# Performance work log

Measured on AMD Instinct MI355X. Metric: run time of the kernel, lower is better.

The kernel has to match this reference:

```python
import math
import jax, jax.numpy as jnp
import numpy as np

B, Q, HID = 4, 4, 4096
NH, NKV, HD = 32, 8, 128
GROUPS = NH // NKV
CACHE_LEN = 4096
CACHE_MAX = CACHE_LEN + 512  # prefill_len + max_len(512)
ROPE_THETA = 500000.0
SCALE = 1.0 / math.sqrt(128.0)  # hardcoded softmax_scale in module


def rotate_half(x):
    x1, x2 = jnp.split(x, 2, axis=-1)
    return jnp.concatenate([-x2, x1], axis=-1)


def setup_inputs() -> dict:
    key = jax.random.key(0)
    ks = jax.random.split(key, 8)
    std = 0.02
    # RoPE angles for positions [CACHE_LEN, CACHE_LEN+Q)
    pos = (CACHE_LEN + jnp.arange(Q)).astype(jnp.float32)
    inv_freq = 1.0 / (ROPE_THETA ** (jnp.arange(0, HD, 2, dtype=jnp.float32) / HD))
    freqs = pos[:, None] * inv_freq[None, :]            # [Q, HD/2]
    emb = jnp.concatenate([freqs, freqs], axis=-1)      # [Q, HD]
    cos = jnp.broadcast_to(jnp.cos(emb)[None], (B, Q, HD)).astype(jnp.float32)
    sin = jnp.broadcast_to(jnp.sin(emb)[None], (B, Q, HD)).astype(jnp.float32)
    return {
        "hidden_states": jax.random.normal(ks[0], (B, Q, HID), jnp.float32),
        "cos": cos,
        "sin": sin,
        "K_Cache": jax.random.normal(ks[1], (B, NKV, CACHE_MAX, HD), jnp.float32) * 0.5,
        "V_Cache": jax.random.normal(ks[2], (B, NKV, CACHE_MAX, HD), jnp.float32) * 0.5,
        "Wq": jax.random.normal(ks[3], (NH * HD, HID), jnp.float32) * std,
        "Wk": jax.random.normal(ks[4], (NKV * HD, HID), jnp.float32) * std,
        "Wv": jax.random.normal(ks[5], (NKV * HD, HID), jnp.float32) * std,
        "Wo": jax.random.normal(ks[6], (HID, NH * HD), jnp.float32) * std,
        "cache_lens": int(CACHE_LEN),
    }


def reference(hidden_states, cos, sin, K_Cache, V_Cache, Wq, Wk, Wv, Wo, cache_lens):
    b, q, _ = hidden_states.shape
    # projections (torch Linear: x @ W.T), reshape to [b, h, q, d]
    qs = jnp.einsum('bsh,oh->bso', hidden_states, Wq).reshape(b, q, NH, HD).transpose(0, 2, 1, 3)
    ks = jnp.einsum('bsh,oh->bso', hidden_states, Wk).reshape(b, q, NKV, HD).transpose(0, 2, 1, 3)
    vs = jnp.einsum('bsh,oh->bso', hidden_states, Wv).reshape(b, q, NKV, HD).transpose(0, 2, 1, 3)
    # RoPE, unsqueeze_dim=1 (head axis)
    c, s = cos[:, None, :, :], sin[:, None, :, :]
    qs = qs * c + rotate_half(qs) * s
    ks = ks * c + rotate_half(ks) * s
    # scatter new K/V into the cache at offset cache_lens
    K_Cache = K_Cache.at[:, :, cache_lens:cache_lens + q, :].set(ks)
    V_Cache = V_Cache.at[:, :, cache_lens:cache_lens + q, :].set(vs)
    # K_total/V_total = cache prefix ++ fresh keys/values; GQA repeat
    K_total = jnp.repeat(jnp.concatenate([K_Cache[:, :, :cache_lens, :], ks], axis=2), GROUPS, axis=1)
    V_total = jnp.repeat(jnp.concatenate([V_Cache[:, :, :cache_lens, :], vs], axis=2), GROUPS, axis=1)
    scores = jnp.einsum('bhqd,bhkd->bhqk', qs, K_total) * SCALE
    # causal mask over the appended q tokens, cache prefix fully visible
    tri = jnp.triu(jnp.ones((q, q), bool), 1)
    mask = jnp.concatenate([jnp.zeros((q, cache_lens), bool), tri], axis=1)
    scores = jnp.where(mask[None, None], -jnp.inf, scores)
    attn = jax.nn.softmax(scores.astype(jnp.float32), axis=-1).astype(V_total.dtype)
    out = jnp.einsum('bhqk,bhkd->bhqd', attn, V_total)
    out = out.transpose(0, 2, 1, 3).reshape(b, q, NH * HD)
    return jnp.einsum('bsh,oh->bso', out, Wo)
```

## Files before the change

### kernel.cpp

```cpp
#include <hip/hip_runtime.h>
#include <math.h>

#define HIDK 4096
#define NHQ 32
#define HD 128
#define CMAX 4608
#define CLEN 4096
#define NCH 32
#define SCALE 0.08838834764831845f

__device__ __forceinline__ float4 ld4(const float* p) { return *reinterpret_cast<const float4*>(p); }
__device__ __forceinline__ float dot4(float4 a, float4 b) { return a.x*b.x + a.y*b.y + a.z*b.z + a.w*b.w; }
__device__ __forceinline__ int swz(int row, int colf) { return row * 128 + (colf ^ ((row & 31) << 2)); }

__global__ __launch_bounds__(256) void gemm3_kernel(
    const float* __restrict__ X,
    const float* __restrict__ W1, const float* __restrict__ W2, const float* __restrict__ W3,
    int n1, int n2,
    float* __restrict__ o1, int os1,
    float* __restrict__ o2, int os2,
    float* __restrict__ o3, int os3)
{
  __shared__ float Xs[2][16][256];

  const int tid = threadIdx.x, lane = tid & 63, w = tid >> 6;
  const int o = blockIdx.x * 8 + w * 2;

  const float* Wb; float* ob; int os;
  if (o < n1)           { Wb = W1 + (size_t)o * HIDK;            ob = o1 + o;            os = os1; }
  else if (o < n1 + n2) { const int f = o - n1;      Wb = W2 + (size_t)f * HIDK; ob = o2 + f; os = os2; }
  else                  { const int f = o - n1 - n2; Wb = W3 + (size_t)f * HIDK; ob = o3 + f; os = os3; }

  const int xr = tid >> 6;
  const int sr = tid >> 4;
  (void)xr; (void)sr;

  const int strow = tid >> 6;
  const int stcol = (tid & 63) * 4;

  float acc0[16], acc1[16];
  #pragma unroll
  for (int b = 0; b < 16; ++b) { acc0[b] = 0.f; acc1[b] = 0.f; }

  #pragma unroll
  for (int j = 0; j < 4; ++j)
    *(float4*)&Xs[0][strow + j * 4][stcol] = ld4(X + (size_t)(strow + j * 4) * HIDK + stcol);

  int cur = 0;
  #pragma unroll 2
  for (int kt = 0; kt < 16; ++kt) {
    const float4 w0 = ld4(Wb + (size_t)kt * 256 + lane * 4);
    const float4 w1 = ld4(Wb + HIDK + (size_t)kt * 256 + lane * 4);
    float4 g[4];
    if (kt < 15) {
      #pragma unroll
      for (int j = 0; j < 4; ++j)
        g[j] = ld4(X + (size_t)(strow + j * 4) * HIDK + (kt + 1) * 256 + stcol);
    }
    __syncthreads();
    #pragma unroll
    for (int b = 0; b < 16; ++b) {
      const float4 x4 = *(const float4*)&Xs[cur][b][lane * 4];
      acc0[b] += dot4(x4, w0);
      acc1[b] += dot4(x4, w1);
    }
    if (kt < 15) {
      #pragma unroll
      for (int j = 0; j < 4; ++j)
        *(float4*)&Xs[cur ^ 1][strow + j * 4][stcol] = g[j];
    }
    cur ^= 1;
  }

  #pragma unroll
  for (int m = 1; m < 64; m <<= 1)
    #pragma unroll
    for (int b = 0; b < 16; ++b) {
      acc0[b] += __shfl_xor(acc0[b], m, 64);
      acc1[b] += __shfl_xor(acc1[b], m, 64);
    }
  if (lane == 0) {
    #pragma unroll
    for (int b = 0; b < 16; ++b) {
      ob[(size_t)b * os]     = acc0[b];
      ob[(size_t)b * os + 1] = acc1[b];
    }
  }
}

__global__ __launch_bounds__(256) void attn2_kernel(
    const float* __restrict__ qraw, const float* __restrict__ Kc, const float* __restrict__ Vc,
    const float* __restrict__ cosp, const float* __restrict__ sinp,
    float* __restrict__ partO, float* __restrict__ partM, float* __restrict__ partL)
{
  __shared__ float qsh[16][128];
  __shared__ float KV[64 * 128];
  __shared__ float P[128][20];

  const int tid = threadIdx.x, lane = tid & 63, w = tid >> 6;
  const int chunk = blockIdx.x & 31, bkv = blockIdx.x >> 5;
  const int b = bkv >> 3, kv = bkv & 7;
  const int p0 = chunk * 128;

  const float* Kbase = Kc + ((size_t)(b * 8 + kv) * CMAX + p0) * HD;
  const float* Vbase = Vc + ((size_t)(b * 8 + kv) * CMAX + p0) * HD;
  const int c0 = (tid & 31) * 4, r0 = tid >> 5;

  #pragma unroll
  for (int j = 0; j < 8; ++j) {
    const int e = tid + j * 256;
    const int r = e >> 7, d = e & 127;
    const int s = r & 3, hl = r >> 2;
    const float* qp = qraw + (size_t)(b * 4 + s) * HIDK + (kv * 4 + hl) * HD;
    const float c  = cosp[(b * 4 + s) * HD + d];
    const float sn = sinp[(b * 4 + s) * HD + d];
    const float sgn = (d < 64) ? -1.f : 1.f;
    qsh[r][d] = (qp[d] * c + sgn * qp[d ^ 64] * sn) * SCALE;
  }
  #pragma unroll
  for (int j = 0; j < 8; ++j) {
    const int r = r0 + j * 8;
    *(float4*)&KV[swz(r, c0)] = ld4(Kbase + (size_t)r * HD + c0);
  }
  __syncthreads();

  const int pos16 = lane & 15, quart = lane >> 4;
  const int prow = w * 16 + pos16;

  #pragma unroll
  for (int t = 0; t < 2; ++t) {
    float sc[16];
    #pragma unroll
    for (int r = 0; r < 16; ++r) sc[r] = 0.f;
    #pragma unroll
    for (int d4 = 0; d4 < 8; ++d4) {
      const int kcol = quart * 32 + d4 * 4;
      const float4 k4 = *(const float4*)&KV[swz(prow, kcol)];
      #pragma unroll
      for (int r = 0; r < 16; ++r)
        sc[r] += dot4(k4, *(const float4*)&qsh[r][kcol]);
    }
    #pragma unroll
    for (int r = 0; r < 16; ++r) {
      sc[r] += __shfl_xor(sc[r], 16, 64);
      sc[r] += __shfl_xor(sc[r], 32, 64);
    }
    if (lane < 16) {
      #pragma unroll
      for (int r = 0; r < 16; ++r) P[t * 64 + prow][r] = sc[r];
    }
    __syncthreads();
    if (t == 0) {
      #pragma unroll
      for (int j = 0; j < 8; ++j) {
        const int r = r0 + j * 8;
        *(float4*)&KV[swz(r, c0)] = ld4(Kbase + (size_t)(64 + r) * HD + c0);
      }
      __syncthreads();
    }
  }

  float4 g[8];
  #pragma unroll
  for (int j = 0; j < 8; ++j)
    g[j] = ld4(Vbase + (size_t)(r0 + j * 8) * HD + c0);

  #pragma unroll
  for (int rr = 0; rr < 4; ++rr) {
    const int r = w * 4 + rr;
    float v0 = P[lane][r], v1 = P[lane + 64][r];
    float mx = fmaxf(v0, v1);
    #pragma unroll
    for (int m = 1; m < 64; m <<= 1) mx = fmaxf(mx, __shfl_xor(mx, m, 64));
    v0 = __expf(v0 - mx);
    v1 = __expf(v1 - mx);
    P[lane][r] = v0;
    P[lane + 64][r] = v1;
    float l = v0 + v1;
    #pragma unroll
    for (int m = 1; m < 64; m <<= 1) l += __shfl_xor(l, m, 64);
    if (lane == 0) {
      const int row = (b * NHQ + kv * 4 + (r >> 2)) * 4 + (r & 3);
      partM[row * NCH + chunk] = mx;
      partL[row * NCH + chunk] = l;
    }
  }
  #pragma unroll
  for (int j = 0; j < 8; ++j)
    *(float4*)&KV[swz(r0 + j * 8, c0)] = g[j];
  __syncthreads();

  const int ph = lane >> 5, vc0 = (lane & 31) * 4;
  float4 o[4];
  #pragma unroll
  for (int rr = 0; rr < 4; ++rr) o[rr] = make_float4(0.f, 0.f, 0.f, 0.f);

  #pragma unroll
  for (int t = 0; t < 2; ++t) {
    #pragma unroll 4
    for (int i = 0; i < 32; ++i) {
      const int pr = 2 * i + ph;
      const float4 v4 = *(const float4*)&KV[swz(pr, vc0)];
      const float4 p4 = *(const float4*)&P[t * 64 + pr][w * 4];
      o[0].x += p4.x * v4.x; o[0].y += p4.x * v4.y; o[0].z += p4.x * v4.z; o[0].w += p4.x * v4.w;
      o[1].x += p4.y * v4.x; o[1].y += p4.y * v4.y; o[1].z += p4.y * v4.z; o[1].w += p4.y * v4.w;
      o[2].x += p4.z * v4.x; o[2].y += p4.z * v4.y; o[2].z += p4.z * v4.z; o[2].w += p4.z * v4.w;
      o[3].x += p4.w * v4.x; o[3].y += p4.w * v4.y; o[3].z += p4.w * v4.z; o[3].w += p4.w * v4.w;
    }
    if (t == 0) {
      __syncthreads();
      #pragma unroll
      for (int j = 0; j < 8; ++j) {
        const int r = r0 + j * 8;
        *(float4*)&KV[swz(r, c0)] = ld4(Vbase + (size_t)(64 + r) * HD + c0);
      }
      __syncthreads();
    }
  }

  #pragma unroll
  for (int rr = 0; rr < 4; ++rr) {
    o[rr].x += __shfl_xor(o[rr].x, 32, 64);
    o[rr].y += __shfl_xor(o[rr].y, 32, 64);
    o[rr].z += __shfl_xor(o[rr].z, 32, 64);
    o[rr].w += __shfl_xor(o[rr].w, 32, 64);
  }
  if (lane < 32) {
    #pragma unroll
    for (int rr = 0; rr < 4; ++rr) {
      const int r = w * 4 + rr;
      const int row = (b * NHQ + kv * 4 + (r >> 2)) * 4 + (r & 3);
      *(float4*)&partO[((size_t)row * NCH + chunk) * HD + lane * 4] = o[rr];
    }
  }
}

__global__ __launch_bounds__(64) void combine_kernel(
    const float* __restrict__ qraw, const float* __restrict__ kraw, const float* __restrict__ vraw,
    const float* __restrict__ cosp, const float* __restrict__ sinp,
    const float* __restrict__ partO, const float* __restrict__ partM, const float* __restrict__ partL,
    float* __restrict__ attn)
{
  const int bid = blockIdx.x;
  const int s = bid & 3;
  const int h = (bid >> 2) & 31;
  const int b = bid >> 7;
  const int kv = h >> 2;
  const int lane = threadIdx.x;
  const int d0 = lane * 2;

  float M = -INFINITY;
  #pragma unroll 4
  for (int c = 0; c < NCH; ++c) M = fmaxf(M, partM[bid * NCH + c]);

  float qr0, qr1;
  {
    const float* qp = qraw + (size_t)(b * 4 + s) * HIDK + h * HD;
    const float c0 = cosp[(b * 4 + s) * HD + d0],     sn0 = sinp[(b * 4 + s) * HD + d0];
    const float c1 = cosp[(b * 4 + s) * HD + d0 + 1], sn1 = sinp[(b * 4 + s) * HD + d0 + 1];
    const float sg0 = (d0 < 64) ? -1.f : 1.f;
    const float sg1 = ((d0 + 1) < 64) ? -1.f : 1.f;
    qr0 = (qp[d0] * c0 + sg0 * qp[d0 ^ 64] * sn0) * SCALE;
    qr1 = (qp[d0 + 1] * c1 + sg1 * qp[(d0 + 1) ^ 64] * sn1) * SCALE;
  }

  float sj[4] = {0.f, 0.f, 0.f, 0.f};
  float Mp = M;
  #pragma unroll
  for (int j = 0; j < 4; ++j) {
    if (j <= s) {
      const float* kp = kraw + (size_t)(b * 4 + j) * 1024 + kv * HD;
      const float c0 = cosp[(b * 4 + j) * HD + d0],     sn0 = sinp[(b * 4 + j) * HD + d0];
      const float c1 = cosp[(b * 4 + j) * HD + d0 + 1], sn1 = sinp[(b * 4 + j) * HD + d0 + 1];
      const float sg0 = (d0 < 64) ? -1.f : 1.f;
      const float sg1 = ((d0 + 1) < 64) ? -1.f : 1.f;
      const float kr0 = kp[d0] * c0 + sg0 * kp[d0 ^ 64] * sn0;
      const float kr1 = kp[d0 + 1] * c1 + sg1 * kp[(d0 + 1) ^ 64] * sn1;
      float part = qr0 * kr0 + qr1 * kr1;
      #pragma unroll
      for (int m = 1; m < 64; m <<= 1) part += __shfl_xor(part, m, 64);
      sj[j] = part;
      Mp = fmaxf(Mp, part);
    }
  }

  float ltot = 0.f, O0 = 0.f, O1 = 0.f;
  #pragma unroll 4
  for (int c = 0; c < NCH; ++c) {
    const float a = __expf(partM[bid * NCH + c] - Mp);
    ltot += partL[bid * NCH + c] * a;
    const float2 v = *(const float2*)&partO[((size_t)bid * NCH + c) * HD + d0];
    O0 += a * v.x;
    O1 += a * v.y;
  }
  #pragma unroll
  for (int j = 0; j < 4; ++j) {
    if (j <= s) {
      const float e = __expf(sj[j] - Mp);
      ltot += e;
      const float* vp = vraw + (size_t)(b * 4 + j) * 1024 + kv * HD + d0;
      O0 += e * vp[0];
      O1 += e * vp[1];
    }
  }
  const float inv = 1.f / ltot;
  *(float2*)&attn[(size_t)(b * 4 + s) * HIDK + h * HD + d0] = make_float2(O0 * inv, O1 * inv);
}

extern "C" void kernel_launch(void* const* d_in, const int* in_sizes, int n_in,
                              void* d_out, int out_size, void* d_ws, size_t ws_size,
                              hipStream_t stream)
{
  const float* hid  = (const float*)d_in[0];
  const float* cosp = (const float*)d_in[1];
  const float* sinp = (const float*)d_in[2];
  const float* Kc   = (const float*)d_in[3];
  const float* Vc   = (const float*)d_in[4];
  const float* Wq   = (const float*)d_in[5];
  const float* Wk   = (const float*)d_in[6];
  const float* Wv   = (const float*)d_in[7];
  const float* Wo   = (const float*)d_in[8];
  float* out = (float*)d_out;

  float* ws    = (float*)d_ws;
  float* qraw  = ws;
  float* kraw  = ws + 65536;
  float* vraw  = ws + 81920;
  float* attn  = ws + 98304;
  float* partO = ws + 163840;
  float* partM = partO + (size_t)512 * NCH * 128;
  float* partL = partM + (size_t)512 * NCH;

  gemm3_kernel<<<768, 256, 0, stream>>>(hid, Wq, Wk, Wv, 4096, 1024,
                                        qraw, 4096, kraw, 1024, vraw, 1024);
  attn2_kernel<<<32 * NCH, 256, 0, stream>>>(qraw, Kc, Vc, cosp, sinp, partO, partM, partL);
  combine_kernel<<<512, 64, 0, stream>>>(qraw, kraw, vraw, cosp, sinp, partO, partM, partL, attn);
  gemm3_kernel<<<512, 256, 0, stream>>>(attn, Wo, Wo, Wo, 4096, 0,
                                        out, 4096, out, 4096, out, 4096);
}
```

Measured before the change: 136.3 us.

## Stream K/V directly from global in split-KV attention, prep rotated Q separately

Replaces the LDS-staged attention kernel with one where each wave reads K rows and V rows straight from global memory and keeps 16 query rows in registers. RoPE on Q moves into a separate prep kernel that writes a transposed, pre-scaled Q for broadcast reads, and the two waves merge their softmax partials in LDS. Partial outputs are stored in fp16 to halve partO traffic into the combine kernel. The costs are an extra launch, higher register pressure from 16 float4 accumulators, and reduced precision in the partial outputs.

```diff
diff --git a/kernel.cpp b/kernel.cpp
--- a/kernel.cpp
+++ b/kernel.cpp
@@ -1,4 +1,5 @@
 #include <hip/hip_runtime.h>
+#include <hip/hip_fp16.h>
 #include <math.h>
 
 #define HIDK 4096
@@ -11,7 +12,6 @@
 
 __device__ __forceinline__ float4 ld4(const float* p) { return *reinterpret_cast<const float4*>(p); }
 __device__ __forceinline__ float dot4(float4 a, float4 b) { return a.x*b.x + a.y*b.y + a.z*b.z + a.w*b.w; }
-__device__ __forceinline__ int swz(int row, int colf) { return row * 128 + (colf ^ ((row & 31) << 2)); }
 
 __global__ __launch_bounds__(256) void gemm3_kernel(
     const float* __restrict__ X,
@@ -31,10 +31,6 @@
   else if (o < n1 + n2) { const int f = o - n1;      Wb = W2 + (size_t)f * HIDK; ob = o2 + f; os = os2; }
   else                  { const int f = o - n1 - n2; Wb = W3 + (size_t)f * HIDK; ob = o3 + f; os = os3; }
 
-  const int xr = tid >> 6;
-  const int sr = tid >> 4;
-  (void)xr; (void)sr;
-
   const int strow = tid >> 6;
   const int stcol = (tid & 63) * 4;
 
@@ -88,157 +84,129 @@
   }
 }
 
-__global__ __launch_bounds__(256) void attn2_kernel(
-    const float* __restrict__ qraw, const float* __restrict__ Kc, const float* __restrict__ Vc,
-    const float* __restrict__ cosp, const float* __restrict__ sinp,
-    float* __restrict__ partO, float* __restrict__ partM, float* __restrict__ partL)
-{
-  __shared__ float qsh[16][128];
-  __shared__ float KV[64 * 128];
-  __shared__ float P[128][20];
+__global__ __launch_bounds__(256) void qt_prep_kernel(
+    const float* __restrict__ qraw, const float* __restrict__ cosp,
+    const float* __restrict__ sinp, float* __restrict__ qt)
+{
+  const int e = blockIdx.x * 256 + threadIdx.x;
+  const int r = e & 15;
+  const int d = (e >> 4) & 127;
+  const int bkv = e >> 11;
+  const int b = bkv >> 3, kv = bkv & 7;
+  const int s = r & 3, hl = r >> 2;
+  const float* qp = qraw + (size_t)(b * 4 + s) * HIDK + (kv * 4 + hl) * HD;
+  const float c  = cosp[(b * 4 + s) * HD + d];
+  const float sn = sinp[(b * 4 + s) * HD + d];
+  const float sgn = (d < 64) ? -1.f : 1.f;
+  qt[e] = (qp[d] * c + sgn * qp[d ^ 64] * sn) * SCALE;
+}
+
+__global__ __launch_bounds__(128) void attn3_kernel(
+    const float* __restrict__ qt, const float* __restrict__ Kc, const float* __restrict__ Vc,
+    __half* __restrict__ partOh, float* __restrict__ partM, float* __restrict__ partL)
+{
+  __shared__ float Plds[2][16][66];
+  __shared__ float Oex[16][132];
+  __shared__ float MLe[32];
 
   const int tid = threadIdx.x, lane = tid & 63, w = tid >> 6;
   const int chunk = blockIdx.x & 31, bkv = blockIdx.x >> 5;
   const int b = bkv >> 3, kv = bkv & 7;
-  const int p0 = chunk * 128;
-
-  const float* Kbase = Kc + ((size_t)(b * 8 + kv) * CMAX + p0) * HD;
-  const float* Vbase = Vc + ((size_t)(b * 8 + kv) * CMAX + p0) * HD;
-  const int c0 = (tid & 31) * 4, r0 = tid >> 5;
-
-  #pragma unroll
-  for (int j = 0; j < 8; ++j) {
-    const int e = tid + j * 256;
-    const int r = e >> 7, d = e & 127;
-    const int s = r & 3, hl = r >> 2;
-    const float* qp = qraw + (size_t)(b * 4 + s) * HIDK + (kv * 4 + hl) * HD;
-    const float c  = cosp[(b * 4 + s) * HD + d];
-    const float sn = sinp[(b * 4 + s) * HD + d];
-    const float sgn = (d < 64) ? -1.f : 1.f;
-    qsh[r][d] = (qp[d] * c + sgn * qp[d ^ 64] * sn) * SCALE;
-  }
-  #pragma unroll
-  for (int j = 0; j < 8; ++j) {
-    const int r = r0 + j * 8;
-    *(float4*)&KV[swz(r, c0)] = ld4(Kbase + (size_t)r * HD + c0);
+  const int p0 = chunk * 128 + w * 64;
+
+  const float* qtb = qt + (size_t)bkv * 2048;
+  const float* Kp  = Kc + ((size_t)bkv * CMAX + p0 + lane) * HD;
+
+  float sc[16];
+  #pragma unroll
+  for (int r = 0; r < 16; ++r) sc[r] = 0.f;
+  #pragma unroll 4
+  for (int d4 = 0; d4 < 32; ++d4) {
+    const float4 k4 = ld4(Kp + d4 * 4);
+    #pragma unroll
+    for (int r = 0; r < 16; ++r) sc[r] += k4.x * qtb[(d4 * 4 + 0) * 16 + r];
+    #pragma unroll
+    for (int r = 0; r < 16; ++r) sc[r] += k4.y * qtb[(d4 * 4 + 1) * 16 + r];
+    #pragma unroll
+    for (int r = 0; r < 16; ++r) sc[r] += k4.z * qtb[(d4 * 4 + 2) * 16 + r];
+    #pragma unroll
+    for (int r = 0; r < 16; ++r) sc[r] += k4.w * qtb[(d4 * 4 + 3) * 16 + r];
+  }
+
+  float m[16], l[16];
+  #pragma unroll
+  for (int r = 0; r < 16; ++r) {
+    float mx = sc[r];
+    #pragma unroll
+    for (int st = 1; st < 64; st <<= 1) mx = fmaxf(mx, __shfl_xor(mx, st, 64));
+    const float p = __expf(sc[r] - mx);
+    float ls = p;
+    #pragma unroll
+    for (int st = 1; st < 64; st <<= 1) ls += __shfl_xor(ls, st, 64);
+    m[r] = mx; l[r] = ls;
+    Plds[w][r][lane] = p;
+  }
+
+  const int dsub = lane & 31, par = lane >> 5;
+  const float* Vp = Vc + ((size_t)bkv * CMAX + p0 + par) * HD + dsub * 4;
+  float4 o[16];
+  #pragma unroll
+  for (int r = 0; r < 16; ++r) o[r] = make_float4(0.f, 0.f, 0.f, 0.f);
+  #pragma unroll 4
+  for (int i = 0; i < 32; ++i) {
+    const float4 v4 = ld4(Vp + (size_t)(2 * i) * HD);
+    #pragma unroll
+    for (int r = 0; r < 16; ++r) {
+      const float p = Plds[w][r][2 * i + par];
+      o[r].x += p * v4.x; o[r].y += p * v4.y; o[r].z += p * v4.z; o[r].w += p * v4.w;
+    }
+  }
+  #pragma unroll
+  for (int r = 0; r < 16; ++r) {
+    o[r].x += __shfl_xor(o[r].x, 32, 64);
+    o[r].y += __shfl_xor(o[r].y, 32, 64);
+    o[r].z += __shfl_xor(o[r].z, 32, 64);
+    o[r].w += __shfl_xor(o[r].w, 32, 64);
+  }
+
+  if (w == 1) {
+    if (lane < 32) {
+      #pragma unroll
+      for (int r = 0; r < 16; ++r) *(float4*)&Oex[r][dsub * 4] = o[r];
+    }
+    if (lane == 0) {
+      #pragma unroll
+      for (int r = 0; r < 16; ++r) { MLe[r] = m[r]; MLe[16 + r] = l[r]; }
+    }
   }
   __syncthreads();
-
-  const int pos16 = lane & 15, quart = lane >> 4;
-  const int prow = w * 16 + pos16;
-
-  #pragma unroll
-  for (int t = 0; t < 2; ++t) {
-    float sc[16];
-    #pragma unroll
-    for (int r = 0; r < 16; ++r) sc[r] = 0.f;
-    #pragma unroll
-    for (int d4 = 0; d4 < 8; ++d4) {
-      const int kcol = quart * 32 + d4 * 4;
-      const float4 k4 = *(const float4*)&KV[swz(prow, kcol)];
-      #pragma unroll
-      for (int r = 0; r < 16; ++r)
-        sc[r] += dot4(k4, *(const float4*)&qsh[r][kcol]);
-    }
+  if (w == 0 && lane < 32) {
     #pragma unroll
     for (int r = 0; r < 16; ++r) {
-      sc[r] += __shfl_xor(sc[r], 16, 64);
-      sc[r] += __shfl_xor(sc[r], 32, 64);
-    }
-    if (lane < 16) {
-      #pragma unroll
-      for (int r = 0; r < 16; ++r) P[t * 64 + prow][r] = sc[r];
-    }
-    __syncthreads();
-    if (t == 0) {
-      #pragma unroll
-      for (int j = 0; j < 8; ++j) {
-        const int r = r0 + j * 8;
-        *(float4*)&KV[swz(r, c0)] = ld4(Kbase + (size_t)(64 + r) * HD + c0);
+      const float m1 = MLe[r], l1 = MLe[16 + r];
+      const float M  = fmaxf(m[r], m1);
+      const float a0 = __expf(m[r] - M), a1 = __expf(m1 - M);
+      const float4 o1 = *(const float4*)&Oex[r][dsub * 4];
+      const float ox = a0 * o[r].x + a1 * o1.x;
+      const float oy = a0 * o[r].y + a1 * o1.y;
+      const float oz = a0 * o[r].z + a1 * o1.z;
+      const float ow = a0 * o[r].w + a1 * o1.w;
+      const int row = (b * NHQ + kv * 4 + (r >> 2)) * 4 + (r & 3);
+      const size_t idx = ((size_t)row * NCH + chunk) * HD + dsub * 4;
+      *(__half2*)&partOh[idx]     = __floats2half2_rn(ox, oy);
+      *(__half2*)&partOh[idx + 2] = __floats2half2_rn(oz, ow);
+      if (dsub == 0) {
+        partM[row * NCH + chunk] = M;
+        partL[row * NCH + chunk] = a0 * l[r] + a1 * l1;
       }
-      __syncthreads();
-    }
-  }
-
-  float4 g[8];
-  #pragma unroll
-  for (int j = 0; j < 8; ++j)
-    g[j] = ld4(Vbase + (size_t)(r0 + j * 8) * HD + c0);
-
-  #pragma unroll
-  for (int rr = 0; rr < 4; ++rr) {
-    const int r = w * 4 + rr;
-    float v0 = P[lane][r], v1 = P[lane + 64][r];
-    float mx = fmaxf(v0, v1);
-    #pragma unroll
-    for (int m = 1; m < 64; m <<= 1) mx = fmaxf(mx, __shfl_xor(mx, m, 64));
-    v0 = __expf(v0 - mx);
-    v1 = __expf(v1 - mx);
-    P[lane][r] = v0;
-    P[lane + 64][r] = v1;
-    float l = v0 + v1;
-    #pragma unroll
-    for (int m = 1; m < 64; m <<= 1) l += __shfl_xor(l, m, 64);
-    if (lane == 0) {
-      const int row = (b * NHQ + kv * 4 + (r >> 2)) * 4 + (r & 3);
-      partM[row * NCH + chunk] = mx;
-      partL[row * NCH + chunk] = l;
-    }
-  }
-  #pragma unroll
-  for (int j = 0; j < 8; ++j)
-    *(float4*)&KV[swz(r0 + j * 8, c0)] = g[j];
-  __syncthreads();
-
-  const int ph = lane >> 5, vc0 = (lane & 31) * 4;
-  float4 o[4];
-  #pragma unroll
-  for (int rr = 0; rr < 4; ++rr) o[rr] = make_float4(0.f, 0.f, 0.f, 0.f);
-
-  #pragma unroll
-  for (int t = 0; t < 2; ++t) {
-    #pragma unroll 4
-    for (int i = 0; i < 32; ++i) {
-      const int pr = 2 * i + ph;
-      const float4 v4 = *(const float4*)&KV[swz(pr, vc0)];
-      const float4 p4 = *(const float4*)&P[t * 64 + pr][w * 4];
-      o[0].x += p4.x * v4.x; o[0].y += p4.x * v4.y; o[0].z += p4.x * v4.z; o[0].w += p4.x * v4.w;
-      o[1].x += p4.y * v4.x; o[1].y += p4.y * v4.y; o[1].z += p4.y * v4.z; o[1].w += p4.y * v4.w;
-      o[2].x += p4.z * v4.x; o[2].y += p4.z * v4.y; o[2].z += p4.z * v4.z; o[2].w += p4.z * v4.w;
-      o[3].x += p4.w * v4.x; o[3].y += p4.w * v4.y; o[3].z += p4.w * v4.z; o[3].w += p4.w * v4.w;
-    }
-    if (t == 0) {
-      __syncthreads();
-      #pragma unroll
-      for (int j = 0; j < 8; ++j) {
-        const int r = r0 + j * 8;
-        *(float4*)&KV[swz(r, c0)] = ld4(Vbase + (size_t)(64 + r) * HD + c0);
-      }
-      __syncthreads();
-    }
-  }
-
-  #pragma unroll
-  for (int rr = 0; rr < 4; ++rr) {
-    o[rr].x += __shfl_xor(o[rr].x, 32, 64);
-    o[rr].y += __shfl_xor(o[rr].y, 32, 64);
-    o[rr].z += __shfl_xor(o[rr].z, 32, 64);
-    o[rr].w += __shfl_xor(o[rr].w, 32, 64);
-  }
-  if (lane < 32) {
-    #pragma unroll
-    for (int rr = 0; rr < 4; ++rr) {
-      const int r = w * 4 + rr;
-      const int row = (b * NHQ + kv * 4 + (r >> 2)) * 4 + (r & 3);
-      *(float4*)&partO[((size_t)row * NCH + chunk) * HD + lane * 4] = o[rr];
     }
   }
 }
 
 __global__ __launch_bounds__(64) void combine_kernel(
-    const float* __restrict__ qraw, const float* __restrict__ kraw, const float* __restrict__ vraw,
+    const float* __restrict__ qt, const float* __restrict__ kraw, const float* __restrict__ vraw,
     const float* __restrict__ cosp, const float* __restrict__ sinp,
-    const float* __restrict__ partO, const float* __restrict__ partM, const float* __restrict__ partL,
+    const __half* __restrict__ partOh, const float* __restrict__ partM, const float* __restrict__ partL,
     float* __restrict__ attn)
 {
   const int bid = blockIdx.x;
@@ -253,16 +221,9 @@
   #pragma unroll 4
   for (int c = 0; c < NCH; ++c) M = fmaxf(M, partM[bid * NCH + c]);
 
-  float qr0, qr1;
-  {
-    const float* qp = qraw + (size_t)(b * 4 + s) * HIDK + h * HD;
-    const float c0 = cosp[(b * 4 + s) * HD + d0],     sn0 = sinp[(b * 4 + s) * HD + d0];
-    const float c1 = cosp[(b * 4 + s) * HD + d0 + 1], sn1 = sinp[(b * 4 + s) * HD + d0 + 1];
-    const float sg0 = (d0 < 64) ? -1.f : 1.f;
-    const float sg1 = ((d0 + 1) < 64) ? -1.f : 1.f;
-    qr0 = (qp[d0] * c0 + sg0 * qp[d0 ^ 64] * sn0) * SCALE;
-    qr1 = (qp[d0 + 1] * c1 + sg1 * qp[(d0 + 1) ^ 64] * sn1) * SCALE;
-  }
+  const int rloc = (h & 3) * 4 + s;
+  const float qr0 = qt[((size_t)(b * 8 + kv) * 128 + d0) * 16 + rloc];
+  const float qr1 = qt[((size_t)(b * 8 + kv) * 128 + d0 + 1) * 16 + rloc];
 
   float sj[4] = {0.f, 0.f, 0.f, 0.f};
   float Mp = M;
@@ -289,7 +250,7 @@
   for (int c = 0; c < NCH; ++c) {
     const float a = __expf(partM[bid * NCH + c] - Mp);
     ltot += partL[bid * NCH + c] * a;
-    const float2 v = *(const float2*)&partO[((size_t)bid * NCH + c) * HD + d0];
+    const float2 v = __half22float2(*(const __half2*)&partOh[((size_t)bid * NCH + c) * HD + d0]);
     O0 += a * v.x;
     O1 += a * v.y;
   }
@@ -323,18 +284,21 @@
   float* out = (float*)d_out;
 
   float* ws    = (float*)d_ws;
-  float* qraw  = ws;
-  float* kraw  = ws + 65536;
-  float* vraw  = ws + 81920;
-  float* attn  = ws + 98304;
-  float* partO = ws + 163840;
-  float* partM = partO + (size_t)512 * NCH * 128;
-  float* partL = partM + (size_t)512 * NCH;
+  float*  kraw   = ws;
+  float*  vraw   = ws + 16384;
+  float*  attn   = ws + 32768;
+  float*  qt     = ws + 98304;
+  float*  qraw   = ws + 163840;
+  float*  partM  = ws + 229376;
+  float*  partL  = ws + 245760;
+  __half* partOh = (__half*)(ws + 262144);
 
   gemm3_kernel<<<768, 256, 0, stream>>>(hid, Wq, Wk, Wv, 4096, 1024,
                                         qraw, 4096, kraw, 1024, vraw, 1024);
-  attn2_kernel<<<32 * NCH, 256, 0, stream>>>(qraw, Kc, Vc, cosp, sinp, partO, partM, partL);
-  combine_kernel<<<512, 64, 0, stream>>>(qraw, kraw, vraw, cosp, sinp, partO, partM, partL, attn);
+  qt_prep_kernel<<<256, 256, 0, stream>>>(qraw, cosp, sinp, qt);
+  attn3_kernel<<<1024, 128, 0, stream>>>(qt, Kc, Vc, partOh, partM, partL);
+  combine_kernel<<<512, 64, 0, stream>>>(qt, kraw, vraw, cosp, sinp,
+                                         partOh, partM, partL, attn);
   gemm3_kernel<<<512, 256, 0, stream>>>(attn, Wo, Wo, Wo, 4096, 0,
                                         out, 4096, out, 4096, out, 4096);
 }
```

After: 121.4 us. 11.0% less time.
